# Performance work log

Measured on AMD Instinct MI355X. Metric: run time of the kernel, lower is better.

The kernel has to match this reference:

```python
import jax, jax.numpy as jnp
from jax import lax
import numpy as np

THRESHOLD = 0.8
SECONDARY = 0.6
SECONDARY_WEIGHT = 0.5
BN_EPS = 1e-5


def _conv_relu_pool(x, W, b):
    # x: [B,C,H,W], W: [O,I,3,3]
    y = lax.conv_general_dilated(x, W, window_strides=(1, 1), padding='SAME',
                                 dimension_numbers=('NCHW', 'OIHW', 'NCHW'))
    y = y + b[None, :, None, None]
    y = jax.nn.relu(y)
    return lax.reduce_window(y, -jnp.inf, lax.max, (1, 1, 2, 2), (1, 1, 2, 2), 'VALID')


def setup_inputs() -> dict:
    key = jax.random.key(0)
    ks = jax.random.split(key, 12)
    B, H, W = 1024, 64, 64
    d0, d1, d2 = 4096, 1024, 256  # qnn_arch
    inp = {}
    inp['x'] = jax.random.normal(ks[0], (B, 1, H, W), dtype=jnp.float32)
    # conv params (kaiming-ish scaling)
    inp['cw1'] = jax.random.normal(ks[1], (8, 1, 3, 3), jnp.float32) * (1.0 / np.sqrt(1 * 9))
    inp['cb1'] = jax.random.normal(ks[2], (8,), jnp.float32) * 0.01
    inp['cw2'] = jax.random.normal(ks[3], (16, 8, 3, 3), jnp.float32) * (1.0 / np.sqrt(8 * 9))
    inp['cb2'] = jax.random.normal(ks[4], (16,), jnp.float32) * 0.01
    # linear layers of the 'graph QNN'
    inp['w1'] = jax.random.normal(ks[5], (d1, d0), jnp.float32) * (1.0 / np.sqrt(d0))
    inp['b1'] = jax.random.normal(ks[6], (d1,), jnp.float32) * 0.01
    inp['w2'] = jax.random.normal(ks[7], (d2, d1), jnp.float32) * (1.0 / np.sqrt(d1))
    inp['b2'] = jax.random.normal(ks[8], (d2,), jnp.float32) * 0.01
    # BatchNorm1d affine params
    inp['gamma'] = jnp.ones((d2,), jnp.float32)
    inp['beta'] = jnp.zeros((d2,), jnp.float32)
    return inp


def reference(x, cw1, cb1, cw2, cb2, w1, b1, w2, b2, gamma, beta):
    B = x.shape[0]
    # CNN feature extractor
    feat = _conv_relu_pool(x, cw1, cb1)
    feat = _conv_relu_pool(feat, cw2, cb2)
    flat = feat.reshape(B, -1)                      # [B, 4096]
    # graph-QNN layers with tanh
    h1 = jnp.tanh(flat @ w1.T + b1)                 # [B, 1024]
    last = jnp.tanh(h1 @ w2.T + b2)                 # [B, 256]
    # fidelity adjacency: vectorized normalize + Gram + squared cosine
    norms = jnp.linalg.norm(last, axis=1, keepdims=True)  # [B,1]
    nrm = last / (norms + 1e-12)
    fid = (nrm @ nrm.T) ** 2                        # [B, B]
    adj = jnp.where(fid >= THRESHOLD, 1.0,
                    jnp.where(fid >= SECONDARY, SECONDARY_WEIGHT, 0.0))
    adj = adj * (1.0 - jnp.eye(B, dtype=adj.dtype))  # no self-edges
    # BatchNorm1d (training mode: batch statistics, biased variance)
    mean = jnp.mean(last, axis=0)
    var = jnp.mean((last - mean) ** 2, axis=0)
    out = (last - mean) / jnp.sqrt(var + BN_EPS) * gamma + beta
    return out, adj
```

## Files before the change

kernel.cpp:

```cpp
#include <hip/hip_runtime.h>
#include <hip/hip_bf16.h>
#include <math.h>


__global__ __launch_bounds__(256) void conv1_kernel(
    const float* __restrict__ x, const float* __restrict__ cw1,
    const float* __restrict__ cb1, float* __restrict__ feat1) {
  __shared__ float sX[66 * 66];
  __shared__ float sW1[72];
  __shared__ float sB1[8];

  const int b = blockIdx.x;
  const int t = threadIdx.x;

  for (int i = t; i < 66 * 66; i += 256) sX[i] = 0.0f;
  if (t < 72) sW1[t] = cw1[t];
  if (t < 8)  sB1[t] = cb1[t];
  __syncthreads();

  const float* xb = x + (size_t)b * 4096;
  for (int i = t; i < 4096; i += 256)
    sX[((i >> 6) + 1) * 66 + (i & 63) + 1] = xb[i];
  __syncthreads();

  for (int task = t; task < 2048; task += 256) {
    const int ch = task >> 8;
    const int rem = task & 255;
    const int py = rem >> 3;
    const int px0 = (rem & 7) * 4;

    double w9[9];
#pragma unroll
    for (int k = 0; k < 9; ++k) w9[k] = (double)sW1[ch * 9 + k];

    float reg[4][10];
#pragma unroll
    for (int r = 0; r < 4; ++r)
#pragma unroll
      for (int c = 0; c < 5; ++c) {
        const float2 v =
            *(const float2*)&sX[(2 * py + r) * 66 + 2 * px0 + 2 * c];
        reg[r][2 * c] = v.x;
        reg[r][2 * c + 1] = v.y;
      }

    float out4[4];
#pragma unroll
    for (int px = 0; px < 4; ++px) {
      double best = -1e300;
#pragma unroll
      for (int dy = 0; dy < 2; ++dy) {
#pragma unroll
        for (int dx = 0; dx < 2; ++dx) {
          double s = 0.0;
#pragma unroll
          for (int ky = 0; ky < 3; ++ky)
#pragma unroll
            for (int kx = 0; kx < 3; ++kx)
              s = fma((double)reg[dy + ky][2 * px + dx + kx], w9[ky * 3 + kx],
                      s);
          best = fmax(best, s);
        }
      }
      out4[px] = (float)fmax(best + (double)sB1[ch], 0.0);
    }
    *(float4*)&feat1[(size_t)b * 8192 + ch * 1024 + py * 32 + px0] =
        make_float4(out4[0], out4[1], out4[2], out4[3]);
  }
}

__global__ __launch_bounds__(256) void conv2_kernel(
    const float* __restrict__ feat1, const float* __restrict__ cw2,
    const float* __restrict__ cb2, float* __restrict__ flat) {
  __shared__ float sF[8 * 34 * 34];
  __shared__ float sW2[1152];
  __shared__ float sB2[16];

  const int b = blockIdx.x;
  const int t = threadIdx.x;

  for (int i = t; i < 8 * 34 * 34; i += 256) sF[i] = 0.0f;
  for (int i = t; i < 1152; i += 256) sW2[i] = cw2[i];
  if (t < 16) sB2[t] = cb2[t];
  __syncthreads();

  const float* fb = feat1 + (size_t)b * 8192;
  for (int i = t; i < 8192; i += 256) {
    const int ch = i >> 10, pos = i & 1023;
    sF[ch * 1156 + ((pos >> 5) + 1) * 34 + (pos & 31) + 1] = fb[i];
  }
  __syncthreads();

  const int py = t >> 4, px = t & 15;
  float* ob = flat + (size_t)b * 4096 + py * 16 + px;

#pragma unroll 1
  for (int oh = 0; oh < 2; ++oh) {
    double acc[8][4];
#pragma unroll
    for (int o = 0; o < 8; ++o)
#pragma unroll
      for (int q = 0; q < 4; ++q) acc[o][q] = 0.0;

#pragma unroll
    for (int ic = 0; ic < 8; ++ic) {
      float r[4][4];
#pragma unroll
      for (int iy = 0; iy < 4; ++iy) {
        const float2 v0 =
            *(const float2*)&sF[ic * 1156 + (2 * py + iy) * 34 + 2 * px];
        const float2 v1 =
            *(const float2*)&sF[ic * 1156 + (2 * py + iy) * 34 + 2 * px + 2];
        r[iy][0] = v0.x; r[iy][1] = v0.y; r[iy][2] = v1.x; r[iy][3] = v1.y;
      }
#pragma unroll
      for (int o = 0; o < 8; ++o) {
        const float* w = &sW2[(oh * 8 + o) * 72 + ic * 9];
        double w9[9];
#pragma unroll
        for (int k = 0; k < 9; ++k) w9[k] = (double)w[k];
#pragma unroll
        for (int dy = 0; dy < 2; ++dy)
#pragma unroll
          for (int dx = 0; dx < 2; ++dx) {
            double s = acc[o][dy * 2 + dx];
#pragma unroll
            for (int ky = 0; ky < 3; ++ky)
#pragma unroll
              for (int kx = 0; kx < 3; ++kx)
                s = fma((double)r[dy + ky][dx + kx], w9[ky * 3 + kx], s);
            acc[o][dy * 2 + dx] = s;
          }
      }
    }
#pragma unroll
    for (int o = 0; o < 8; ++o) {
      const int oc = oh * 8 + o;
      const double best =
          fmax(fmax(acc[o][0], acc[o][1]), fmax(acc[o][2], acc[o][3]));
      ob[oc * 256] = (float)fmax(best + (double)sB2[oc], 0.0);
    }
  }
}

__global__ __launch_bounds__(256) void conv_fused(
    const float* __restrict__ x,
    const float* __restrict__ cw1, const float* __restrict__ cb1,
    const float* __restrict__ cw2, const float* __restrict__ cb2,
    float* __restrict__ flat) {
  __shared__ float sX[66 * 66];
  __shared__ float sF[8 * 34 * 34];
  __shared__ float sW1[72];
  __shared__ float sW2[1152];
  __shared__ float sB1[8];
  __shared__ float sB2[16];

  const int b = blockIdx.x;
  const int t = threadIdx.x;

  for (int i = t; i < 66 * 66; i += 256) sX[i] = 0.0f;
  for (int i = t; i < 8 * 34 * 34; i += 256) sF[i] = 0.0f;
  if (t < 72) sW1[t] = cw1[t];
  for (int i = t; i < 1152; i += 256) sW2[i] = cw2[i];
  if (t < 8)  sB1[t] = cb1[t];
  if (t < 16) sB2[t] = cb2[t];
  __syncthreads();

  const float* xb = x + (size_t)b * 4096;
  for (int i = t; i < 4096; i += 256)
    sX[((i >> 6) + 1) * 66 + (i & 63) + 1] = xb[i];
  __syncthreads();

  for (int p = t; p < 8192; p += 256) {
    const int ch = p >> 10, pos = p & 1023;
    const int py1 = pos >> 5, px1 = pos & 31;
    double best = -1e300;
#pragma unroll
    for (int dy = 0; dy < 2; ++dy)
#pragma unroll
      for (int dx = 0; dx < 2; ++dx) {
        const int y = 2 * py1 + dy, xx = 2 * px1 + dx;
        double s = 0.0;
#pragma unroll
        for (int ky = 0; ky < 3; ++ky)
#pragma unroll
          for (int kx = 0; kx < 3; ++kx)
            s = fma((double)sX[(y + ky) * 66 + xx + kx],
                    (double)sW1[ch * 9 + ky * 3 + kx], s);
        best = fmax(best, s);
      }
    sF[ch * 1156 + (py1 + 1) * 34 + px1 + 1] =
        (float)fmax(best + (double)sB1[ch], 0.0);
  }
  __syncthreads();

  const int py = t >> 4, px = t & 15;
  for (int oh = 0; oh < 2; ++oh) {
    double acc[8][4];
#pragma unroll
    for (int o = 0; o < 8; ++o)
#pragma unroll
      for (int q = 0; q < 4; ++q) acc[o][q] = 0.0;
#pragma unroll
    for (int ic = 0; ic < 8; ++ic) {
      double r[4][4];
#pragma unroll
      for (int iy = 0; iy < 4; ++iy)
#pragma unroll
        for (int ix = 0; ix < 4; ++ix)
          r[iy][ix] = (double)sF[ic * 1156 + (2 * py + iy) * 34 + 2 * px + ix];
#pragma unroll
      for (int o = 0; o < 8; ++o) {
        const float* w = &sW2[(oh * 8 + o) * 72 + ic * 9];
        double w9[9];
#pragma unroll
        for (int k = 0; k < 9; ++k) w9[k] = (double)w[k];
#pragma unroll
        for (int dy = 0; dy < 2; ++dy)
#pragma unroll
          for (int dx = 0; dx < 2; ++dx) {
            double s = acc[o][dy * 2 + dx];
#pragma unroll
            for (int ky = 0; ky < 3; ++ky)
#pragma unroll
              for (int kx = 0; kx < 3; ++kx)
                s = fma(r[dy + ky][dx + kx], w9[ky * 3 + kx], s);
            acc[o][dy * 2 + dx] = s;
          }
      }
    }
    float* ob = flat + (size_t)b * 4096 + py * 16 + px;
#pragma unroll
    for (int o = 0; o < 8; ++o) {
      const int oc = oh * 8 + o;
      double best =
          fmax(fmax(acc[o][0], acc[o][1]), fmax(acc[o][2], acc[o][3]));
      ob[oc * 256] = (float)fmax(best + (double)sB2[oc], 0.0);
    }
  }
}

__global__ __launch_bounds__(256) void gemm_nt_f64_v3(
    const float* __restrict__ A, const float* __restrict__ B,
    double* __restrict__ P, int M, int N, int K, int Kc) {
  __shared__ double As[16][130];
  __shared__ double Bs[16][130];

  const int t = threadIdx.x;
  const int n0 = blockIdx.x * 128;
  const int m0 = blockIdx.y * 128;
  const int s  = blockIdx.z;
  const int kb = s * Kc;
  const int rS = t >> 2;
  const int cS = (t & 3) * 4;
  const int ty = t >> 4;
  const int tx = t & 15;

  double acc[8][8];
#pragma unroll
  for (int i = 0; i < 8; ++i)
#pragma unroll
    for (int j = 0; j < 8; ++j) acc[i][j] = 0.0;

  const float* Alo = &A[(size_t)(m0 + rS) * K + cS];
  const float* Ahi = &A[(size_t)(m0 + 64 + rS) * K + cS];
  const float* Blo = &B[(size_t)(n0 + rS) * K + cS];
  const float* Bhi = &B[(size_t)(n0 + 64 + rS) * K + cS];

  float4 a0 = *(const float4*)&Alo[kb];
  float4 a1 = *(const float4*)&Ahi[kb];
  float4 b0 = *(const float4*)&Blo[kb];
  float4 b1 = *(const float4*)&Bhi[kb];

  for (int k0 = kb; k0 < kb + Kc; k0 += 16) {
    __syncthreads();
    As[cS + 0][rS] = (double)a0.x; As[cS + 1][rS] = (double)a0.y;
    As[cS + 2][rS] = (double)a0.z; As[cS + 3][rS] = (double)a0.w;
    As[cS + 0][64 + rS] = (double)a1.x; As[cS + 1][64 + rS] = (double)a1.y;
    As[cS + 2][64 + rS] = (double)a1.z; As[cS + 3][64 + rS] = (double)a1.w;
    Bs[cS + 0][rS] = (double)b0.x; Bs[cS + 1][rS] = (double)b0.y;
    Bs[cS + 2][rS] = (double)b0.z; Bs[cS + 3][rS] = (double)b0.w;
    Bs[cS + 0][64 + rS] = (double)b1.x; Bs[cS + 1][64 + rS] = (double)b1.y;
    Bs[cS + 2][64 + rS] = (double)b1.z; Bs[cS + 3][64 + rS] = (double)b1.w;
    if (k0 + 16 < kb + Kc) {
      a0 = *(const float4*)&Alo[k0 + 16];
      a1 = *(const float4*)&Ahi[k0 + 16];
      b0 = *(const float4*)&Blo[k0 + 16];
      b1 = *(const float4*)&Bhi[k0 + 16];
    }
    __syncthreads();
#pragma unroll
    for (int k = 0; k < 16; ++k) {
      double ar[8], br[8];
#pragma unroll
      for (int g = 0; g < 4; ++g) {
        const double2 av = *(const double2*)&As[k][32 * g + 2 * ty];
        ar[2 * g] = av.x; ar[2 * g + 1] = av.y;
        const double2 bv = *(const double2*)&Bs[k][32 * g + 2 * tx];
        br[2 * g] = bv.x; br[2 * g + 1] = bv.y;
      }
#pragma unroll
      for (int i = 0; i < 8; ++i)
#pragma unroll
        for (int j = 0; j < 8; ++j)
          acc[i][j] = fma(ar[i], br[j], acc[i][j]);
    }
  }

  double* Pp = P + (size_t)s * M * N;
#pragma unroll
  for (int i = 0; i < 8; ++i) {
    const int row = m0 + 32 * (i >> 1) + 2 * ty + (i & 1);
#pragma unroll
    for (int h = 0; h < 4; ++h) {
      const int col = n0 + 32 * h + 2 * tx;
      *(double2*)&Pp[(size_t)row * N + col] =
          make_double2(acc[i][2 * h], acc[i][2 * h + 1]);
    }
  }
}

__global__ __launch_bounds__(256) void reduce_tanh(
    const double* __restrict__ P, int S, const float* __restrict__ bias,
    float* __restrict__ C, int N, int total) {
  const int idx = blockIdx.x * 256 + threadIdx.x;
  if (idx >= total) return;
  double sum = 0.0;
  for (int s = 0; s < S; ++s) sum += P[(size_t)s * total + idx];
  const float zg = (float)sum;
  const float z = zg + bias[idx % N];
  C[idx] = (float)tanh((double)z);
}

__global__ __launch_bounds__(256) void reduce_tanh_norm(
    const double* __restrict__ P, int S, const float* __restrict__ bias,
    float* __restrict__ last, float* __restrict__ nrm) {
  const int b = blockIdx.x;
  const int t = threadIdx.x;
  const int idx = b * 256 + t;
  const int total = 1024 * 256;
  double sum = 0.0;
  for (int s = 0; s < S; ++s) sum += P[(size_t)s * total + idx];
  const float zg = (float)sum;
  const float z = zg + bias[t];
  const float v = (float)tanh((double)z);
  last[idx] = v;

  const float sq = v * v;
  double s = (double)sq;
#pragma unroll
  for (int o = 32; o > 0; o >>= 1) s += __shfl_down(s, o);
  __shared__ double red[4];
  if ((t & 63) == 0) red[t >> 6] = s;
  __syncthreads();
  const double totalSq = red[0] + red[1] + red[2] + red[3];
  const float s32 = (float)totalSq;
  const float den = sqrtf(s32) + 1e-12f;
  nrm[idx] = v / den;
}

__global__ __launch_bounds__(256) void gram_adj_direct(
    const float* __restrict__ Nrm, float* __restrict__ adj, int Msz, int K) {
  __shared__ double As[16][66];
  __shared__ double Bs[16][66];

  const int t = threadIdx.x;
  const int n0 = blockIdx.x * 64;
  const int m0 = blockIdx.y * 64;
  const int lm = t >> 2;
  const int lk4 = (t & 3) * 4;
  const int ty = t >> 4;
  const int tx = t & 15;

  double acc[4][4];
#pragma unroll
  for (int i = 0; i < 4; ++i)
#pragma unroll
    for (int j = 0; j < 4; ++j) acc[i][j] = 0.0;

  for (int k0 = 0; k0 < K; k0 += 16) {
    const float4 av = *(const float4*)&Nrm[(size_t)(m0 + lm) * K + k0 + lk4];
    const float4 bv = *(const float4*)&Nrm[(size_t)(n0 + lm) * K + k0 + lk4];
    __syncthreads();
    As[lk4 + 0][lm] = (double)av.x; As[lk4 + 1][lm] = (double)av.y;
    As[lk4 + 2][lm] = (double)av.z; As[lk4 + 3][lm] = (double)av.w;
    Bs[lk4 + 0][lm] = (double)bv.x; Bs[lk4 + 1][lm] = (double)bv.y;
    Bs[lk4 + 2][lm] = (double)bv.z; Bs[lk4 + 3][lm] = (double)bv.w;
    __syncthreads();
#pragma unroll
    for (int k = 0; k < 16; ++k) {
      const double2 a01 = *(const double2*)&As[k][2 * ty];
      const double2 a23 = *(const double2*)&As[k][32 + 2 * ty];
      const double2 b01 = *(const double2*)&Bs[k][2 * tx];
      const double2 b23 = *(const double2*)&Bs[k][32 + 2 * tx];
      const double ar[4] = {a01.x, a01.y, a23.x, a23.y};
      const double br[4] = {b01.x, b01.y, b23.x, b23.y};
#pragma unroll
      for (int i = 0; i < 4; ++i)
#pragma unroll
        for (int j = 0; j < 4; ++j)
          acc[i][j] = fma(ar[i], br[j], acc[i][j]);
    }
  }

  const int rows[4] = {m0 + 2 * ty, m0 + 2 * ty + 1,
                       m0 + 32 + 2 * ty, m0 + 32 + 2 * ty + 1};
  const int cols[4] = {n0 + 2 * tx, n0 + 2 * tx + 1,
                       n0 + 32 + 2 * tx, n0 + 32 + 2 * tx + 1};
#pragma unroll
  for (int i = 0; i < 4; ++i)
#pragma unroll
    for (int j = 0; j < 4; ++j) {
      const float g = (float)acc[i][j];
      const float fid = g * g;
      float v = (fid >= 0.8f) ? 1.0f : ((fid >= 0.6f) ? 0.5f : 0.0f);
      if (rows[i] == cols[j]) v = 0.0f;
      adj[(size_t)rows[i] * Msz + cols[j]] = v;
    }
}

__global__ __launch_bounds__(256) void bn_stats(
    const float* __restrict__ last, const float* __restrict__ gamma,
    const float* __restrict__ beta, float* __restrict__ out) {
  const int j = blockIdx.x;
  const int t = threadIdx.x;
  double v[4];
  double s = 0.0;
#pragma unroll
  for (int i = 0; i < 4; ++i) {
    v[i] = (double)last[(size_t)(i * 256 + t) * 256 + j];
    s += v[i];
  }
#pragma unroll
  for (int o = 32; o > 0; o >>= 1) s += __shfl_down(s, o);
  __shared__ double red[4];
  if ((t & 63) == 0) red[t >> 6] = s;
  __syncthreads();
  const double mean = (red[0] + red[1] + red[2] + red[3]) * (1.0 / 1024.0);
  double q = 0.0;
#pragma unroll
  for (int i = 0; i < 4; ++i) {
    const double d = v[i] - mean;
    q += d * d;
  }
#pragma unroll
  for (int o = 32; o > 0; o >>= 1) q += __shfl_down(q, o);
  __syncthreads();
  if ((t & 63) == 0) red[t >> 6] = q;
  __syncthreads();
  const double var = (red[0] + red[1] + red[2] + red[3]) * (1.0 / 1024.0);
  const double g = (double)gamma[j] / sqrt(var + 1e-5);
  const double be = (double)beta[j];
#pragma unroll
  for (int i = 0; i < 4; ++i)
    out[(size_t)(i * 256 + t) * 256 + j] = (float)((v[i] - mean) * g + be);
}

extern "C" void kernel_launch(void* const* d_in, const int* in_sizes, int n_in,
                              void* d_out, int out_size, void* d_ws,
                              size_t ws_size, hipStream_t stream) {
  const float* x     = (const float*)d_in[0];
  const float* cw1   = (const float*)d_in[1];
  const float* cb1   = (const float*)d_in[2];
  const float* cw2   = (const float*)d_in[3];
  const float* cb2   = (const float*)d_in[4];
  const float* w1    = (const float*)d_in[5];
  const float* b1    = (const float*)d_in[6];
  const float* w2    = (const float*)d_in[7];
  const float* b2    = (const float*)d_in[8];
  const float* gamma = (const float*)d_in[9];
  const float* beta  = (const float*)d_in[10];

  float* outp = (float*)d_out;
  float* adj  = outp + 1024 * 256;

  float* ws   = (float*)d_ws;
  float* flat = ws;
  float* h1   = ws + 4194304;
  float* last = ws + 5242880;
  float* nrm  = ws + 5505024;
  double* part = (double*)(ws + 5767168);
  float* feat1 = (float*)part;

  const size_t baseB = 5767168ull * 4ull;
  int S1;
  if (ws_size >= baseB + 16ull * 1024 * 1024 * 8) S1 = 16;
  else if (ws_size >= baseB + 8ull * 1024 * 1024 * 8) S1 = 8;
  else if (ws_size >= baseB + 4ull * 1024 * 1024 * 8) S1 = 4;
  else S1 = 2;
  const int S2 = (S1 >= 4) ? 16 : 4;
  const bool split_conv = (S1 >= 4);

  if (split_conv) {
    conv1_kernel<<<1024, 256, 0, stream>>>(x, cw1, cb1, feat1);
    conv2_kernel<<<1024, 256, 0, stream>>>(feat1, cw2, cb2, flat);
  } else {
    conv_fused<<<1024, 256, 0, stream>>>(x, cw1, cb1, cw2, cb2, flat);
  }

  gemm_nt_f64_v3<<<dim3(8, 8, S1), 256, 0, stream>>>(
      flat, w1, part, 1024, 1024, 4096, 4096 / S1);
  reduce_tanh<<<4096, 256, 0, stream>>>(part, S1, b1, h1, 1024, 1024 * 1024);

  gemm_nt_f64_v3<<<dim3(2, 8, S2), 256, 0, stream>>>(
      h1, w2, part, 1024, 256, 1024, 1024 / S2);
  reduce_tanh_norm<<<1024, 256, 0, stream>>>(part, S2, b2, last, nrm);

  gram_adj_direct<<<dim3(16, 16), 256, 0, stream>>>(nrm, adj, 1024, 256);

  bn_stats<<<256, 256, 0, stream>>>(last, gamma, beta, outp);
}
```

Measured before the change: 426.7 us.

## Use FP64 MFMA instructions for split-K linear GEMMs with 128x64 tiles

Replaces the scalar FP64 FMA inner loop of the split-K GEMM with __builtin_amdgcn_mfma_f64_16x16x4f64 matrix-core instructions. Each wave computes a 64x32 subtile, and the block tile shrinks from 128x128 to 128x64. The first GEMM's split factor drops from 16 to 8, which halves the partial-sum traffic for the reduce. The aim is to move the dominant FP64 GEMM work onto the matrix cores. The trade-off is scalar epilogue stores and a different accumulation order.

```diff
diff --git a/kernel.cpp b/kernel.cpp
--- a/kernel.cpp
+++ b/kernel.cpp
@@ -2,6 +2,8 @@
 #include <hip/hip_bf16.h>
 #include <math.h>
 
+
+typedef double f64x4 __attribute__((ext_vector_type(4)));
 
 __global__ __launch_bounds__(256) void conv1_kernel(
     const float* __restrict__ x, const float* __restrict__ cw1,
@@ -240,37 +242,39 @@
   }
 }
 
-__global__ __launch_bounds__(256) void gemm_nt_f64_v3(
+__global__ __launch_bounds__(256) void gemm_nt_mfma_f64(
     const float* __restrict__ A, const float* __restrict__ B,
     double* __restrict__ P, int M, int N, int K, int Kc) {
   __shared__ double As[16][130];
-  __shared__ double Bs[16][130];
-
-  const int t = threadIdx.x;
-  const int n0 = blockIdx.x * 128;
+  __shared__ double Bs[16][66];
+
+  const int t = threadIdx.x;
+  const int n0 = blockIdx.x * 64;
   const int m0 = blockIdx.y * 128;
   const int s  = blockIdx.z;
   const int kb = s * Kc;
   const int rS = t >> 2;
   const int cS = (t & 3) * 4;
-  const int ty = t >> 4;
-  const int tx = t & 15;
-
-  double acc[8][8];
-#pragma unroll
-  for (int i = 0; i < 8; ++i)
-#pragma unroll
-    for (int j = 0; j < 8; ++j) acc[i][j] = 0.0;
+  const int w  = t >> 6;
+  const int lane = t & 63;
+  const int lq = lane >> 4;
+  const int ln = lane & 15;
+  const int mW = (w >> 1) * 64;
+  const int nW = (w & 1) * 32;
+
+  f64x4 acc[4][2];
+#pragma unroll
+  for (int g = 0; g < 4; ++g)
+#pragma unroll
+    for (int h = 0; h < 2; ++h) acc[g][h] = {0.0, 0.0, 0.0, 0.0};
 
   const float* Alo = &A[(size_t)(m0 + rS) * K + cS];
   const float* Ahi = &A[(size_t)(m0 + 64 + rS) * K + cS];
-  const float* Blo = &B[(size_t)(n0 + rS) * K + cS];
-  const float* Bhi = &B[(size_t)(n0 + 64 + rS) * K + cS];
+  const float* Bro = &B[(size_t)(n0 + rS) * K + cS];
 
   float4 a0 = *(const float4*)&Alo[kb];
   float4 a1 = *(const float4*)&Ahi[kb];
-  float4 b0 = *(const float4*)&Blo[kb];
-  float4 b1 = *(const float4*)&Bhi[kb];
+  float4 b0 = *(const float4*)&Bro[kb];
 
   for (int k0 = kb; k0 < kb + Kc; k0 += 16) {
     __syncthreads();
@@ -280,42 +284,40 @@
     As[cS + 2][64 + rS] = (double)a1.z; As[cS + 3][64 + rS] = (double)a1.w;
     Bs[cS + 0][rS] = (double)b0.x; Bs[cS + 1][rS] = (double)b0.y;
     Bs[cS + 2][rS] = (double)b0.z; Bs[cS + 3][rS] = (double)b0.w;
-    Bs[cS + 0][64 + rS] = (double)b1.x; Bs[cS + 1][64 + rS] = (double)b1.y;
-    Bs[cS + 2][64 + rS] = (double)b1.z; Bs[cS + 3][64 + rS] = (double)b1.w;
     if (k0 + 16 < kb + Kc) {
       a0 = *(const float4*)&Alo[k0 + 16];
       a1 = *(const float4*)&Ahi[k0 + 16];
-      b0 = *(const float4*)&Blo[k0 + 16];
-      b1 = *(const float4*)&Bhi[k0 + 16];
+      b0 = *(const float4*)&Bro[k0 + 16];
     }
     __syncthreads();
 #pragma unroll
-    for (int k = 0; k < 16; ++k) {
-      double ar[8], br[8];
-#pragma unroll
-      for (int g = 0; g < 4; ++g) {
-        const double2 av = *(const double2*)&As[k][32 * g + 2 * ty];
-        ar[2 * g] = av.x; ar[2 * g + 1] = av.y;
-        const double2 bv = *(const double2*)&Bs[k][32 * g + 2 * tx];
-        br[2 * g] = bv.x; br[2 * g + 1] = bv.y;
-      }
-#pragma unroll
-      for (int i = 0; i < 8; ++i)
-#pragma unroll
-        for (int j = 0; j < 8; ++j)
-          acc[i][j] = fma(ar[i], br[j], acc[i][j]);
+    for (int kq = 0; kq < 4; ++kq) {
+      const int kr = 4 * kq + lq;
+      double aF[4], bF[2];
+#pragma unroll
+      for (int g = 0; g < 4; ++g) aF[g] = As[kr][mW + 16 * g + ln];
+#pragma unroll
+      for (int h = 0; h < 2; ++h) bF[h] = Bs[kr][nW + 16 * h + ln];
+#pragma unroll
+      for (int g = 0; g < 4; ++g)
+#pragma unroll
+        for (int h = 0; h < 2; ++h)
+          acc[g][h] = __builtin_amdgcn_mfma_f64_16x16x4f64(aF[g], bF[h],
+                                                           acc[g][h], 0, 0, 0);
     }
   }
 
   double* Pp = P + (size_t)s * M * N;
 #pragma unroll
-  for (int i = 0; i < 8; ++i) {
-    const int row = m0 + 32 * (i >> 1) + 2 * ty + (i & 1);
-#pragma unroll
-    for (int h = 0; h < 4; ++h) {
-      const int col = n0 + 32 * h + 2 * tx;
-      *(double2*)&Pp[(size_t)row * N + col] =
-          make_double2(acc[i][2 * h], acc[i][2 * h + 1]);
+  for (int g = 0; g < 4; ++g) {
+#pragma unroll
+    for (int h = 0; h < 2; ++h) {
+#pragma unroll
+      for (int v = 0; v < 4; ++v) {
+        const int row = m0 + mW + 16 * g + 4 * lq + v;
+        const int col = n0 + nW + 16 * h + ln;
+        Pp[(size_t)row * N + col] = acc[g][h][v];
+      }
     }
   }
 }
@@ -484,8 +486,7 @@
 
   const size_t baseB = 5767168ull * 4ull;
   int S1;
-  if (ws_size >= baseB + 16ull * 1024 * 1024 * 8) S1 = 16;
-  else if (ws_size >= baseB + 8ull * 1024 * 1024 * 8) S1 = 8;
+  if (ws_size >= baseB + 8ull * 1024 * 1024 * 8) S1 = 8;
   else if (ws_size >= baseB + 4ull * 1024 * 1024 * 8) S1 = 4;
   else S1 = 2;
   const int S2 = (S1 >= 4) ? 16 : 4;
@@ -498,11 +499,11 @@
     conv_fused<<<1024, 256, 0, stream>>>(x, cw1, cb1, cw2, cb2, flat);
   }
 
-  gemm_nt_f64_v3<<<dim3(8, 8, S1), 256, 0, stream>>>(
+  gemm_nt_mfma_f64<<<dim3(16, 8, S1), 256, 0, stream>>>(
       flat, w1, part, 1024, 1024, 4096, 4096 / S1);
   reduce_tanh<<<4096, 256, 0, stream>>>(part, S1, b1, h1, 1024, 1024 * 1024);
 
-  gemm_nt_f64_v3<<<dim3(2, 8, S2), 256, 0, stream>>>(
+  gemm_nt_mfma_f64<<<dim3(4, 8, S2), 256, 0, stream>>>(
       h1, w2, part, 1024, 256, 1024, 1024 / S2);
   reduce_tanh_norm<<<1024, 256, 0, stream>>>(part, S2, b2, last, nrm);
 
```

Result: no change. 426.7 us (+0.0%).
